# Kernel optimization log

Measured on AMD Instinct MI355X. Metric: run time of the kernel, lower is better.

Reference implementation:

```python
import jax, jax.numpy as jnp
import numpy as np


def setup_inputs() -> dict:
    key = jax.random.key(0)
    k1, k2 = jax.random.split(key)
    B, Q, K, H = 8, 2048, 2048, 128
    out_state = jax.random.normal(k1, (B, Q, H), dtype=jnp.float32)
    history = jax.random.normal(k2, (B, K, H), dtype=jnp.float32)
    return {"out_state": out_state, "history": history}


def reference(out_state, history):
    # tanh pre-activation on queries
    q = jnp.tanh(out_state)                              # [B, Q, H]
    # unscaled QK^T scores
    scores = jnp.einsum("bqh,bkh->bqk", q, history)      # [B, Q, K]
    probs = jax.nn.softmax(scores, axis=2)               # softmax over keys
    attn = jnp.einsum("bqk,bkh->bqh", probs, history)    # [B, Q, H]
    return attn
```

## Files before the change

### kernel.cpp

```cpp
#include <hip/hip_runtime.h>
#include <math.h>


typedef _Float16 half8 __attribute__((ext_vector_type(8)));
typedef _Float16 half4 __attribute__((ext_vector_type(4)));
typedef float    f32x4 __attribute__((ext_vector_type(4)));

#define QQ 2048
#define KK 2048
#define HH 128
#define BM 128
#define BN 64
#define NTILES 32
#define NGROUPS 128
#define KS_STR 132
#define VT_STR 68
#define PS_STR 66
#define L2E 1.44269504f
#define SPLITS_MAX 6
#define OSPLIT  ((size_t)NGROUPS * BM * HH)
#define MLSPLIT ((size_t)NGROUPS * BM)

union U32H { unsigned int u; _Float16 h[2]; };

__launch_bounds__(512, 6)
__global__ void attn_main(const float* __restrict__ out_state,
                          const float* __restrict__ history,
                          float* __restrict__ out,
                          float* __restrict__ ws,
                          int splits) {
    __shared__ _Float16 Ks[BN * KS_STR];
    __shared__ _Float16 Vt[HH * VT_STR];
    __shared__ _Float16 Ps[8][16 * PS_STR];

    const int tid  = threadIdx.x;
    const int wave = tid >> 6;
    const int lane = tid & 63;
    const int quad = lane >> 4;
    const int lc   = lane & 15;

    const int bid = blockIdx.x;
    const int s   = bid / NGROUPS;
    const int g   = bid % NGROUPS;
    const int b   = g >> 4;
    const int qb  = g & 15;
    const int m0  = qb * BM;

    const int kt0 = (NTILES * s) / splits;
    const int kt1 = (NTILES * (s + 1)) / splits;

    half8 qf[4];
    {
        const int m = m0 + wave * 16 + lc;
        const float* qrow = out_state + ((size_t)b * QQ + m) * HH;
        #pragma unroll
        for (int s4 = 0; s4 < 4; ++s4) {
            const int h0 = 32 * s4 + quad * 8;
            const float4 a = *(const float4*)(qrow + h0);
            const float4 c = *(const float4*)(qrow + h0 + 4);
            qf[s4][0] = (_Float16)tanhf(a.x); qf[s4][1] = (_Float16)tanhf(a.y);
            qf[s4][2] = (_Float16)tanhf(a.z); qf[s4][3] = (_Float16)tanhf(a.w);
            qf[s4][4] = (_Float16)tanhf(c.x); qf[s4][5] = (_Float16)tanhf(c.y);
            qf[s4][6] = (_Float16)tanhf(c.z); qf[s4][7] = (_Float16)tanhf(c.w);
        }
    }

    const f32x4 zero4 = {0.f, 0.f, 0.f, 0.f};
    f32x4 O[8];
    #pragma unroll
    for (int i = 0; i < 8; ++i) O[i] = zero4;
    f32x4 Osum = zero4;
    float rmax = -3.0e38f;

    const int r0  = tid >> 5;
    const int c4  = (tid & 31) * 4;
    const int h0  = 2 * (tid & 63);
    const int n0t = (tid >> 6) * 8;

    const half8 ones = {(_Float16)1.f,(_Float16)1.f,(_Float16)1.f,(_Float16)1.f,
                        (_Float16)1.f,(_Float16)1.f,(_Float16)1.f,(_Float16)1.f};

    for (int kt = kt0; kt < kt1; ++kt) {
        const int n0 = kt * BN;

        float4 gbuf[4];
        const float* hb = history + ((size_t)b * KK + n0) * HH;
        #pragma unroll
        for (int j = 0; j < 4; ++j)
            gbuf[j] = *(const float4*)(hb + (size_t)(r0 + 16 * j) * HH + c4);

        __syncthreads();
        #pragma unroll
        for (int j = 0; j < 4; ++j) {
            half4 hv;
            hv[0] = (_Float16)gbuf[j].x; hv[1] = (_Float16)gbuf[j].y;
            hv[2] = (_Float16)gbuf[j].z; hv[3] = (_Float16)gbuf[j].w;
            *(half4*)&Ks[(r0 + 16 * j) * KS_STR + c4] = hv;
        }
        __syncthreads();
        {
            half8 ra, rb;
            #pragma unroll
            for (int i = 0; i < 8; ++i) {
                U32H t; t.u = *(const unsigned int*)&Ks[(n0t + i) * KS_STR + h0];
                ra[i] = t.h[0]; rb[i] = t.h[1];
            }
            *(half8*)&Vt[(h0    ) * VT_STR + n0t] = ra;
            *(half8*)&Vt[(h0 + 1) * VT_STR + n0t] = rb;
        }
        __syncthreads();

        f32x4 S[4];
        #pragma unroll
        for (int nt = 0; nt < 4; ++nt) {
            f32x4 acc = zero4;
            #pragma unroll
            for (int s4 = 0; s4 < 4; ++s4) {
                half8 kf = *(half8*)&Ks[(nt * 16 + lc) * KS_STR + 32 * s4 + quad * 8];
                acc = __builtin_amdgcn_mfma_f32_16x16x32_f16(kf, qf[s4], acc, 0, 0, 0);
            }
            S[nt] = acc;
        }

        float tmax = S[0][0];
        #pragma unroll
        for (int nt = 0; nt < 4; ++nt)
            #pragma unroll
            for (int r = 0; r < 4; ++r)
                tmax = fmaxf(tmax, S[nt][r]);
        tmax = fmaxf(tmax, __shfl_xor(tmax, 16, 64));
        tmax = fmaxf(tmax, __shfl_xor(tmax, 32, 64));

        const float nm = fmaxf(rmax, tmax);
        const float alpha = exp2f((rmax - nm) * L2E);
        rmax = nm;

        #pragma unroll
        for (int nt = 0; nt < 4; ++nt)
            #pragma unroll
            for (int r = 0; r < 4; ++r)
                S[nt][r] = exp2f((S[nt][r] - nm) * L2E);

        #pragma unroll
        for (int ct = 0; ct < 8; ++ct) O[ct] *= alpha;
        Osum *= alpha;

        #pragma unroll
        for (int nt = 0; nt < 4; ++nt) {
            half4 pv;
            pv[0] = (_Float16)S[nt][0]; pv[1] = (_Float16)S[nt][1];
            pv[2] = (_Float16)S[nt][2]; pv[3] = (_Float16)S[nt][3];
            *(half4*)&Ps[wave][lc * PS_STR + nt * 16 + quad * 4] = pv;
        }

        #pragma unroll
        for (int s2 = 0; s2 < 2; ++s2) {
            half8 pb = *(half8*)&Ps[wave][lc * PS_STR + s2 * 32 + quad * 8];
            Osum = __builtin_amdgcn_mfma_f32_16x16x32_f16(ones, pb, Osum, 0, 0, 0);
            #pragma unroll
            for (int ct = 0; ct < 8; ++ct) {
                half8 vf = *(half8*)&Vt[(ct * 16 + lc) * VT_STR + s2 * 32 + quad * 8];
                O[ct] = __builtin_amdgcn_mfma_f32_16x16x32_f16(vf, pb, O[ct], 0, 0, 0);
            }
        }
    }

    if (splits == 1) {
        const float inv = 1.0f / Osum[0];
        float* orow = out + ((size_t)b * QQ + m0 + wave * 16 + lc) * HH;
        #pragma unroll
        for (int ct = 0; ct < 8; ++ct) {
            f32x4 v = O[ct] * inv;
            *(f32x4*)&orow[ct * 16 + quad * 4] = v;
        }
        return;
    }

    const size_t mBase = (size_t)splits * OSPLIT;
    const size_t lBase = mBase + (size_t)splits * MLSPLIT;
    float* po = ws + ((size_t)s * NGROUPS + g) * ((size_t)BM * HH) + (size_t)(wave * 16 + lc) * HH;
    #pragma unroll
    for (int ct = 0; ct < 8; ++ct)
        *(f32x4*)&po[ct * 16 + quad * 4] = O[ct];
    if (quad == 0) {
        const size_t idx = (size_t)(s * NGROUPS + g) * BM + wave * 16 + lc;
        ws[mBase + idx] = rmax;
        ws[lBase + idx] = Osum[0];
    }
}

__global__ void attn_combine(const float* __restrict__ ws,
                             float* __restrict__ out,
                             int splits) {
    const int idx = blockIdx.x * 256 + threadIdx.x;
    const int h4   = (idx & 31) * 4;
    const int rest = idx >> 5;
    const int q    = rest & 2047;
    const int b    = rest >> 11;
    const int g    = b * 16 + (q >> 7);
    const int qr   = q & 127;

    const size_t mBase = (size_t)splits * OSPLIT;
    const size_t lBase = mBase + (size_t)splits * MLSPLIT;

    float ms[SPLITS_MAX];
    float M = -3.0e38f;
    for (int sp = 0; sp < splits; ++sp) {
        ms[sp] = ws[mBase + (size_t)(sp * NGROUPS + g) * BM + qr];
        M = fmaxf(M, ms[sp]);
    }
    float denom = 0.f;
    f32x4 val = {0.f, 0.f, 0.f, 0.f};
    for (int sp = 0; sp < splits; ++sp) {
        const float w = exp2f((ms[sp] - M) * L2E);
        denom += w * ws[lBase + (size_t)(sp * NGROUPS + g) * BM + qr];
        const f32x4 ov = *(const f32x4*)&ws[(size_t)(sp * NGROUPS + g) * ((size_t)BM * HH)
                                            + (size_t)qr * HH + h4];
        val += w * ov;
    }
    const float inv = 1.0f / denom;
    *(f32x4*)&out[((size_t)b * QQ + q) * HH + h4] = val * inv;
}

extern "C" void kernel_launch(void* const* d_in, const int* in_sizes, int n_in,
                              void* d_out, int out_size, void* d_ws, size_t ws_size,
                              hipStream_t stream) {
    const float* out_state = (const float*)d_in[0];
    const float* history   = (const float*)d_in[1];
    float* out = (float*)d_out;
    float* ws  = (float*)d_ws;

    int splits = 1;
    for (int cand = SPLITS_MAX; cand >= 2; --cand) {
        const size_t bytes = (size_t)cand * (OSPLIT + 2 * MLSPLIT) * 4;
        if (ws_size >= bytes) { splits = cand; break; }
    }

    attn_main<<<dim3(NGROUPS * splits), dim3(512), 0, stream>>>(out_state, history, out, ws, splits);
    if (splits > 1)
        attn_combine<<<dim3((8 * QQ * HH / 4) / 256), dim3(256), 0, stream>>>(ws, out, splits);
}
```

Before: 131.9 us.

## Give each wave two 16-row query tiles to reuse K/V fragments

Blocks drop from 512 to 256 threads, and each of the 4 waves now handles 32 query rows as two 16-row sub-tiles. Each K and V fragment read from shared memory then feeds two MFMAs, which halves LDS reads per MFMA. The block index mapping also changes so that batch is the fastest-varying index, which changes how blocks share history tiles in L2. The cost is doubled accumulator and register state per wave, with lower occupancy, and each thread now does twice the tile-staging work.

After: 118.7 us. -10.0%, faster.

```diff
diff --git a/kernel.cpp b/kernel.cpp
--- a/kernel.cpp
+++ b/kernel.cpp
@@ -23,7 +23,7 @@
 
 union U32H { unsigned int u; _Float16 h[2]; };
 
-__launch_bounds__(512, 6)
+__launch_bounds__(256, 3)
 __global__ void attn_main(const float* __restrict__ out_state,
                           const float* __restrict__ history,
                           float* __restrict__ out,
@@ -31,7 +31,7 @@
                           int splits) {
     __shared__ _Float16 Ks[BN * KS_STR];
     __shared__ _Float16 Vt[HH * VT_STR];
-    __shared__ _Float16 Ps[8][16 * PS_STR];
+    __shared__ _Float16 Ps[4][2][16 * PS_STR];
 
     const int tid  = threadIdx.x;
     const int wave = tid >> 6;
@@ -40,42 +40,49 @@
     const int lc   = lane & 15;
 
     const int bid = blockIdx.x;
-    const int s   = bid / NGROUPS;
-    const int g   = bid % NGROUPS;
-    const int b   = g >> 4;
-    const int qb  = g & 15;
+    const int b   = bid & 7;
+    const int t   = bid >> 3;
+    const int qb  = t & 15;
+    const int s   = t >> 4;
+    const int g   = b * 16 + qb;
     const int m0  = qb * BM;
 
     const int kt0 = (NTILES * s) / splits;
     const int kt1 = (NTILES * (s + 1)) / splits;
 
-    half8 qf[4];
+    half8 qfa[4], qfb[4];
     {
-        const int m = m0 + wave * 16 + lc;
-        const float* qrow = out_state + ((size_t)b * QQ + m) * HH;
+        const float* qrowA = out_state + ((size_t)b * QQ + m0 + wave * 32 + lc) * HH;
+        const float* qrowB = qrowA + 16 * HH;
         #pragma unroll
         for (int s4 = 0; s4 < 4; ++s4) {
             const int h0 = 32 * s4 + quad * 8;
-            const float4 a = *(const float4*)(qrow + h0);
-            const float4 c = *(const float4*)(qrow + h0 + 4);
-            qf[s4][0] = (_Float16)tanhf(a.x); qf[s4][1] = (_Float16)tanhf(a.y);
-            qf[s4][2] = (_Float16)tanhf(a.z); qf[s4][3] = (_Float16)tanhf(a.w);
-            qf[s4][4] = (_Float16)tanhf(c.x); qf[s4][5] = (_Float16)tanhf(c.y);
-            qf[s4][6] = (_Float16)tanhf(c.z); qf[s4][7] = (_Float16)tanhf(c.w);
+            float4 a = *(const float4*)(qrowA + h0);
+            float4 c = *(const float4*)(qrowA + h0 + 4);
+            qfa[s4][0] = (_Float16)tanhf(a.x); qfa[s4][1] = (_Float16)tanhf(a.y);
+            qfa[s4][2] = (_Float16)tanhf(a.z); qfa[s4][3] = (_Float16)tanhf(a.w);
+            qfa[s4][4] = (_Float16)tanhf(c.x); qfa[s4][5] = (_Float16)tanhf(c.y);
+            qfa[s4][6] = (_Float16)tanhf(c.z); qfa[s4][7] = (_Float16)tanhf(c.w);
+            a = *(const float4*)(qrowB + h0);
+            c = *(const float4*)(qrowB + h0 + 4);
+            qfb[s4][0] = (_Float16)tanhf(a.x); qfb[s4][1] = (_Float16)tanhf(a.y);
+            qfb[s4][2] = (_Float16)tanhf(a.z); qfb[s4][3] = (_Float16)tanhf(a.w);
+            qfb[s4][4] = (_Float16)tanhf(c.x); qfb[s4][5] = (_Float16)tanhf(c.y);
+            qfb[s4][6] = (_Float16)tanhf(c.z); qfb[s4][7] = (_Float16)tanhf(c.w);
         }
     }
 
     const f32x4 zero4 = {0.f, 0.f, 0.f, 0.f};
-    f32x4 O[8];
+    f32x4 Oa[8], Ob[8];
     #pragma unroll
-    for (int i = 0; i < 8; ++i) O[i] = zero4;
-    f32x4 Osum = zero4;
-    float rmax = -3.0e38f;
+    for (int i = 0; i < 8; ++i) { Oa[i] = zero4; Ob[i] = zero4; }
+    f32x4 OsumA = zero4, OsumB = zero4;
+    float rmaxA = -3.0e38f, rmaxB = -3.0e38f;
 
     const int r0  = tid >> 5;
     const int c4  = (tid & 31) * 4;
     const int h0  = 2 * (tid & 63);
-    const int n0t = (tid >> 6) * 8;
+    const int n0t = (tid >> 6) * 16;
 
     const half8 ones = {(_Float16)1.f,(_Float16)1.f,(_Float16)1.f,(_Float16)1.f,
                         (_Float16)1.f,(_Float16)1.f,(_Float16)1.f,(_Float16)1.f};
@@ -83,109 +90,141 @@
     for (int kt = kt0; kt < kt1; ++kt) {
         const int n0 = kt * BN;
 
-        float4 gbuf[4];
+        float4 gbuf[8];
         const float* hb = history + ((size_t)b * KK + n0) * HH;
         #pragma unroll
-        for (int j = 0; j < 4; ++j)
-            gbuf[j] = *(const float4*)(hb + (size_t)(r0 + 16 * j) * HH + c4);
+        for (int j = 0; j < 8; ++j)
+            gbuf[j] = *(const float4*)(hb + (size_t)(r0 + 8 * j) * HH + c4);
 
         __syncthreads();
         #pragma unroll
-        for (int j = 0; j < 4; ++j) {
+        for (int j = 0; j < 8; ++j) {
             half4 hv;
             hv[0] = (_Float16)gbuf[j].x; hv[1] = (_Float16)gbuf[j].y;
             hv[2] = (_Float16)gbuf[j].z; hv[3] = (_Float16)gbuf[j].w;
-            *(half4*)&Ks[(r0 + 16 * j) * KS_STR + c4] = hv;
+            *(half4*)&Ks[(r0 + 8 * j) * KS_STR + c4] = hv;
         }
         __syncthreads();
         {
-            half8 ra, rb;
+            half8 ra0, ra1, rb0, rb1;
             #pragma unroll
             for (int i = 0; i < 8; ++i) {
-                U32H t; t.u = *(const unsigned int*)&Ks[(n0t + i) * KS_STR + h0];
-                ra[i] = t.h[0]; rb[i] = t.h[1];
-            }
-            *(half8*)&Vt[(h0    ) * VT_STR + n0t] = ra;
-            *(half8*)&Vt[(h0 + 1) * VT_STR + n0t] = rb;
+                U32H t2; t2.u = *(const unsigned int*)&Ks[(n0t + i) * KS_STR + h0];
+                ra0[i] = t2.h[0]; rb0[i] = t2.h[1];
+            }
+            #pragma unroll
+            for (int i = 8; i < 16; ++i) {
+                U32H t2; t2.u = *(const unsigned int*)&Ks[(n0t + i) * KS_STR + h0];
+                ra1[i - 8] = t2.h[0]; rb1[i - 8] = t2.h[1];
+            }
+            *(half8*)&Vt[(h0    ) * VT_STR + n0t    ] = ra0;
+            *(half8*)&Vt[(h0    ) * VT_STR + n0t + 8] = ra1;
+            *(half8*)&Vt[(h0 + 1) * VT_STR + n0t    ] = rb0;
+            *(half8*)&Vt[(h0 + 1) * VT_STR + n0t + 8] = rb1;
         }
         __syncthreads();
 
-        f32x4 S[4];
+        f32x4 Sa[4], Sb[4];
         #pragma unroll
         for (int nt = 0; nt < 4; ++nt) {
-            f32x4 acc = zero4;
+            f32x4 aa = zero4, ab = zero4;
             #pragma unroll
             for (int s4 = 0; s4 < 4; ++s4) {
                 half8 kf = *(half8*)&Ks[(nt * 16 + lc) * KS_STR + 32 * s4 + quad * 8];
-                acc = __builtin_amdgcn_mfma_f32_16x16x32_f16(kf, qf[s4], acc, 0, 0, 0);
-            }
-            S[nt] = acc;
-        }
-
-        float tmax = S[0][0];
+                aa = __builtin_amdgcn_mfma_f32_16x16x32_f16(kf, qfa[s4], aa, 0, 0, 0);
+                ab = __builtin_amdgcn_mfma_f32_16x16x32_f16(kf, qfb[s4], ab, 0, 0, 0);
+            }
+            Sa[nt] = aa; Sb[nt] = ab;
+        }
+
+        float tmaxA = Sa[0][0], tmaxB = Sb[0][0];
         #pragma unroll
         for (int nt = 0; nt < 4; ++nt)
             #pragma unroll
-            for (int r = 0; r < 4; ++r)
-                tmax = fmaxf(tmax, S[nt][r]);
-        tmax = fmaxf(tmax, __shfl_xor(tmax, 16, 64));
-        tmax = fmaxf(tmax, __shfl_xor(tmax, 32, 64));
-
-        const float nm = fmaxf(rmax, tmax);
-        const float alpha = exp2f((rmax - nm) * L2E);
-        rmax = nm;
+            for (int r = 0; r < 4; ++r) {
+                tmaxA = fmaxf(tmaxA, Sa[nt][r]);
+                tmaxB = fmaxf(tmaxB, Sb[nt][r]);
+            }
+        tmaxA = fmaxf(tmaxA, __shfl_xor(tmaxA, 16, 64));
+        tmaxA = fmaxf(tmaxA, __shfl_xor(tmaxA, 32, 64));
+        tmaxB = fmaxf(tmaxB, __shfl_xor(tmaxB, 16, 64));
+        tmaxB = fmaxf(tmaxB, __shfl_xor(tmaxB, 32, 64));
+
+        const float nmA = fmaxf(rmaxA, tmaxA);
+        const float nmB = fmaxf(rmaxB, tmaxB);
+        const float alphaA = exp2f((rmaxA - nmA) * L2E);
+        const float alphaB = exp2f((rmaxB - nmB) * L2E);
+        rmaxA = nmA; rmaxB = nmB;
 
         #pragma unroll
         for (int nt = 0; nt < 4; ++nt)
             #pragma unroll
-            for (int r = 0; r < 4; ++r)
-                S[nt][r] = exp2f((S[nt][r] - nm) * L2E);
-
-        #pragma unroll
-        for (int ct = 0; ct < 8; ++ct) O[ct] *= alpha;
-        Osum *= alpha;
+            for (int r = 0; r < 4; ++r) {
+                Sa[nt][r] = exp2f((Sa[nt][r] - nmA) * L2E);
+                Sb[nt][r] = exp2f((Sb[nt][r] - nmB) * L2E);
+            }
+
+        #pragma unroll
+        for (int ct = 0; ct < 8; ++ct) { Oa[ct] *= alphaA; Ob[ct] *= alphaB; }
+        OsumA *= alphaA; OsumB *= alphaB;
 
         #pragma unroll
         for (int nt = 0; nt < 4; ++nt) {
-            half4 pv;
-            pv[0] = (_Float16)S[nt][0]; pv[1] = (_Float16)S[nt][1];
-            pv[2] = (_Float16)S[nt][2]; pv[3] = (_Float16)S[nt][3];
-            *(half4*)&Ps[wave][lc * PS_STR + nt * 16 + quad * 4] = pv;
+            half4 pva, pvb;
+            pva[0] = (_Float16)Sa[nt][0]; pva[1] = (_Float16)Sa[nt][1];
+            pva[2] = (_Float16)Sa[nt][2]; pva[3] = (_Float16)Sa[nt][3];
+            pvb[0] = (_Float16)Sb[nt][0]; pvb[1] = (_Float16)Sb[nt][1];
+            pvb[2] = (_Float16)Sb[nt][2]; pvb[3] = (_Float16)Sb[nt][3];
+            *(half4*)&Ps[wave][0][lc * PS_STR + nt * 16 + quad * 4] = pva;
+            *(half4*)&Ps[wave][1][lc * PS_STR + nt * 16 + quad * 4] = pvb;
         }
 
         #pragma unroll
         for (int s2 = 0; s2 < 2; ++s2) {
-            half8 pb = *(half8*)&Ps[wave][lc * PS_STR + s2 * 32 + quad * 8];
-            Osum = __builtin_amdgcn_mfma_f32_16x16x32_f16(ones, pb, Osum, 0, 0, 0);
+            half8 pba = *(half8*)&Ps[wave][0][lc * PS_STR + s2 * 32 + quad * 8];
+            half8 pbb = *(half8*)&Ps[wave][1][lc * PS_STR + s2 * 32 + quad * 8];
+            OsumA = __builtin_amdgcn_mfma_f32_16x16x32_f16(ones, pba, OsumA, 0, 0, 0);
+            OsumB = __builtin_amdgcn_mfma_f32_16x16x32_f16(ones, pbb, OsumB, 0, 0, 0);
             #pragma unroll
             for (int ct = 0; ct < 8; ++ct) {
                 half8 vf = *(half8*)&Vt[(ct * 16 + lc) * VT_STR + s2 * 32 + quad * 8];
-                O[ct] = __builtin_amdgcn_mfma_f32_16x16x32_f16(vf, pb, O[ct], 0, 0, 0);
-            }
-        }
-    }
-
+                Oa[ct] = __builtin_amdgcn_mfma_f32_16x16x32_f16(vf, pba, Oa[ct], 0, 0, 0);
+                Ob[ct] = __builtin_amdgcn_mfma_f32_16x16x32_f16(vf, pbb, Ob[ct], 0, 0, 0);
+            }
+        }
+    }
+
+    const int qA = wave * 32 + lc;
     if (splits == 1) {
-        const float inv = 1.0f / Osum[0];
-        float* orow = out + ((size_t)b * QQ + m0 + wave * 16 + lc) * HH;
+        const float invA = 1.0f / OsumA[0];
+        const float invB = 1.0f / OsumB[0];
+        float* orowA = out + ((size_t)b * QQ + m0 + qA) * HH;
+        float* orowB = orowA + 16 * HH;
         #pragma unroll
         for (int ct = 0; ct < 8; ++ct) {
-            f32x4 v = O[ct] * inv;
-            *(f32x4*)&orow[ct * 16 + quad * 4] = v;
+            f32x4 va = Oa[ct] * invA;
+            f32x4 vb = Ob[ct] * invB;
+            *(f32x4*)&orowA[ct * 16 + quad * 4] = va;
+            *(f32x4*)&orowB[ct * 16 + quad * 4] = vb;
         }
         return;
     }
 
     const size_t mBase = (size_t)splits * OSPLIT;
     const size_t lBase = mBase + (size_t)splits * MLSPLIT;
-    float* po = ws + ((size_t)s * NGROUPS + g) * ((size_t)BM * HH) + (size_t)(wave * 16 + lc) * HH;
+    float* poA = ws + ((size_t)s * NGROUPS + g) * ((size_t)BM * HH) + (size_t)qA * HH;
+    float* poB = poA + 16 * HH;
     #pragma unroll
-    for (int ct = 0; ct < 8; ++ct)
-        *(f32x4*)&po[ct * 16 + quad * 4] = O[ct];
+    for (int ct = 0; ct < 8; ++ct) {
+        *(f32x4*)&poA[ct * 16 + quad * 4] = Oa[ct];
+        *(f32x4*)&poB[ct * 16 + quad * 4] = Ob[ct];
+    }
     if (quad == 0) {
-        const size_t idx = (size_t)(s * NGROUPS + g) * BM + wave * 16 + lc;
-        ws[mBase + idx] = rmax;
-        ws[lBase + idx] = Osum[0];
+        const size_t idx = (size_t)(s * NGROUPS + g) * BM + qA;
+        ws[mBase + idx]      = rmaxA;
+        ws[lBase + idx]      = OsumA[0];
+        ws[mBase + idx + 16] = rmaxB;
+        ws[lBase + idx + 16] = OsumB[0];
     }
 }
 
@@ -236,7 +275,7 @@
         if (ws_size >= bytes) { splits = cand; break; }
     }
 
-    attn_main<<<dim3(NGROUPS * splits), dim3(512), 0, stream>>>(out_state, history, out, ws, splits);
+    attn_main<<<dim3(NGROUPS * splits), dim3(256), 0, stream>>>(out_state, history, out, ws, splits);
     if (splits > 1)
         attn_combine<<<dim3((8 * QQ * HH / 4) / 256), dim3(256), 0, stream>>>(ws, out, splits);
 }
```
